# Kernel tuning notes

Hardware: AMD Instinct MI355X
Metric: run time of the kernel (lower is better)

Reference implementation:

```python
import jax, jax.numpy as jnp
import numpy as np

LN_EPS = 1e-5
TOP_K = 2


def _layernorm(x, g, b):
    mu = jnp.mean(x, axis=-1, keepdims=True)
    var = jnp.var(x, axis=-1, keepdims=True)
    return (x - mu) * jax.lax.rsqrt(var + LN_EPS) * g + b


def _moe_layer(x, ln_g, ln_b, Wr, br, We, be):
    # x: [B,T,H]; Wr: [H,E]; We: [E,H,H]; be: [E,H]
    E = Wr.shape[-1]
    z = _layernorm(x, ln_g, ln_b)
    logits = jnp.einsum('bth,he->bte', z, Wr) + br
    probs = jax.nn.softmax(logits, axis=-1)
    # top-k masking + renormalization (top_k < num_experts)
    topv, topi = jax.lax.top_k(probs, TOP_K)                      # [B,T,K]
    mask = (jax.nn.one_hot(topi, E, dtype=probs.dtype) * topv[..., None]).sum(-2)  # [B,T,E]
    w = mask / jnp.clip(mask.sum(-1, keepdims=True), 1e-8)
    # dense all-expert compute (faithful to torch.stack over experts), masked combine
    outs = jnp.einsum('bth,ehd->bted', z, We) + be                # [B,T,E,H]
    mixed = jnp.einsum('bte,bted->btd', w, outs)
    return x + mixed


def setup_inputs() -> dict:
    key = jax.random.key(0)
    B, T, H, E, L = 4, 2048, 3072, 4, 2
    ks = jax.random.split(key, 4)
    s = 1.0 / np.sqrt(H)
    x = jax.random.normal(ks[0], (B, T, H), dtype=jnp.float32)
    ln_g = jnp.ones((L, H), jnp.float32)
    ln_b = jnp.zeros((L, H), jnp.float32)
    Wr = jax.random.normal(ks[1], (L, H, E), jnp.float32) * s
    br = jnp.zeros((L, E), jnp.float32)
    We = jax.random.normal(ks[2], (L, E, H, H), jnp.float32) * s
    be = jnp.zeros((L, E, H), jnp.float32)
    return {"x": x, "ln_g": ln_g, "ln_b": ln_b, "Wr": Wr, "br": br, "We": We, "be": be}


def reference(x, ln_g, ln_b, Wr, br, We, be):
    L = ln_g.shape[0]
    for i in range(L):  # fixed small layer count
        x = _moe_layer(x, ln_g[i], ln_b[i], Wr[i], br[i], We[i], be[i])
    return x
```

## Files before the change

### kernel.cpp

```cpp
#include <hip/hip_runtime.h>
#include <hip/hip_bf16.h>
#include <stdint.h>

#define H 3072
#define EXPERTS 4
#define MTOK 8192
#define LN_EPS 1e-5f
#define FLAG_CAP 1024
#define TAU 0.03f
#define NT_MAX 70

#define BM 128
#define BN 128
#define BK 32

typedef __bf16 bf16;
typedef __bf16 bf16x8 __attribute__((ext_vector_type(8)));
typedef __bf16 bf16x4 __attribute__((ext_vector_type(4)));
typedef float  f32x4  __attribute__((ext_vector_type(4)));

typedef const __attribute__((address_space(1))) unsigned char* gas1p;
typedef __attribute__((address_space(3))) unsigned char* las3p;

__device__ __forceinline__ void gload_lds16(const void* g, void* l) {
    __builtin_amdgcn_global_load_lds((gas1p)g, (las3p)l, 16, 0, 0);
}

__device__ __forceinline__ int pair_a(int b) { return b < 3 ? 0 : (b < 5 ? 1 : 2); }
__device__ __forceinline__ int pair_b(int b) { return b < 3 ? b + 1 : (b < 5 ? b - 1 : 3); }

template <int WLO>
__global__ __launch_bounds__(256) void we_transpose(const float* __restrict__ We,
                                                    bf16* __restrict__ Wt_hi,
                                                    bf16* __restrict__ Wt_lo) {
    __shared__ float tile[64][65];
    const int e  = blockIdx.z;
    const int k0 = blockIdx.y * 64;
    const int n0 = blockIdx.x * 64;
    const int tid = threadIdx.x;

    const float* src = We + ((size_t)e * H + k0) * H + n0;
    const int kl = tid >> 4;
    const int nl = (tid & 15) * 4;
#pragma unroll
    for (int it = 0; it < 4; ++it) {
        float4 v = *(const float4*)(src + (size_t)(kl + it * 16) * H + nl);
        tile[kl + it * 16][nl + 0] = v.x;
        tile[kl + it * 16][nl + 1] = v.y;
        tile[kl + it * 16][nl + 2] = v.z;
        tile[kl + it * 16][nl + 3] = v.w;
    }
    __syncthreads();
    const size_t dbase = ((size_t)e * H + n0) * H + k0;
    const int nl2 = tid >> 4;
    const int kl2 = (tid & 15) * 4;
#pragma unroll
    for (int it = 0; it < 4; ++it) {
        bf16x4 oh, ol;
#pragma unroll
        for (int j = 0; j < 4; ++j) {
            float v = tile[kl2 + j][nl2 + it * 16];
            bf16 hi = (bf16)v;
            oh[j] = hi;
            ol[j] = (bf16)(v - (float)hi);
        }
        const size_t doff = dbase + (size_t)(nl2 + it * 16) * H + kl2;
        *(bf16x4*)(Wt_hi + doff) = oh;
        if (WLO) *(bf16x4*)(Wt_lo + doff) = ol;
    }
}

template <int MODE>
__global__ __launch_bounds__(256) void ln_router_k(const float* __restrict__ xin,
                                                   const float* __restrict__ gamma,
                                                   const float* __restrict__ beta,
                                                   const float* __restrict__ Wr,
                                                   const float* __restrict__ br,
                                                   bf16* __restrict__ z,
                                                   float* __restrict__ wout,
                                                   int* __restrict__ bkt,
                                                   int* __restrict__ bcount,
                                                   int* __restrict__ flags) {
    __shared__ float red[4][4];
    __shared__ float bc[2];

    const int t    = blockIdx.x;
    const int tid  = threadIdx.x;
    const int wid  = tid >> 6;
    const int lane = tid & 63;
    const float* xrow = xin + (size_t)t * H;

    float4 xv[3];
    float s = 0.f;
#pragma unroll
    for (int c = 0; c < 3; ++c) {
        xv[c] = *(const float4*)(xrow + (c * 256 + tid) * 4);
        s += xv[c].x + xv[c].y + xv[c].z + xv[c].w;
    }
#pragma unroll
    for (int off = 32; off; off >>= 1) s += __shfl_down(s, off);
    if (lane == 0) red[wid][0] = s;
    __syncthreads();
    if (tid == 0) bc[0] = (red[0][0] + red[1][0] + red[2][0] + red[3][0]) * (1.f / (float)H);
    __syncthreads();
    const float mu = bc[0];

    float d = 0.f;
#pragma unroll
    for (int c = 0; c < 3; ++c) {
        float dx;
        dx = xv[c].x - mu; d += dx * dx;
        dx = xv[c].y - mu; d += dx * dx;
        dx = xv[c].z - mu; d += dx * dx;
        dx = xv[c].w - mu; d += dx * dx;
    }
#pragma unroll
    for (int off = 32; off; off >>= 1) d += __shfl_down(d, off);
    if (lane == 0) red[wid][1] = d;
    __syncthreads();
    if (tid == 0) {
        float var = (red[0][1] + red[1][1] + red[2][1] + red[3][1]) * (1.f / (float)H);
        bc[1] = 1.f / sqrtf(var + LN_EPS);
    }
    __syncthreads();
    const float rs = bc[1];

    float l0 = 0.f, l1 = 0.f, l2 = 0.f, l3 = 0.f;
    bf16* zrow = z + (size_t)t * H;
#pragma unroll
    for (int c = 0; c < 3; ++c) {
        const int i0 = (c * 256 + tid) * 4;
        float4 gv = *(const float4*)(gamma + i0);
        float4 bv = *(const float4*)(beta + i0);
        float zz[4];
        zz[0] = (xv[c].x - mu) * rs * gv.x + bv.x;
        zz[1] = (xv[c].y - mu) * rs * gv.y + bv.y;
        zz[2] = (xv[c].z - mu) * rs * gv.z + bv.z;
        zz[3] = (xv[c].w - mu) * rs * gv.w + bv.w;
        if (MODE == 0) {
            bf16x4 zb = { (bf16)zz[0], (bf16)zz[1], (bf16)zz[2], (bf16)zz[3] };
            *(bf16x4*)(zrow + i0) = zb;
        }
#pragma unroll
        for (int j = 0; j < 4; ++j) {
            float4 wr = *(const float4*)(Wr + (size_t)(i0 + j) * 4);
            l0 += zz[j] * wr.x; l1 += zz[j] * wr.y;
            l2 += zz[j] * wr.z; l3 += zz[j] * wr.w;
        }
    }
    __syncthreads();
#pragma unroll
    for (int off = 32; off; off >>= 1) {
        l0 += __shfl_down(l0, off);
        l1 += __shfl_down(l1, off);
        l2 += __shfl_down(l2, off);
        l3 += __shfl_down(l3, off);
    }
    if (lane == 0) { red[wid][0] = l0; red[wid][1] = l1; red[wid][2] = l2; red[wid][3] = l3; }
    __syncthreads();
    if (tid == 0) {
        float lf[4];
#pragma unroll
        for (int e = 0; e < 4; ++e)
            lf[e] = red[0][e] + red[1][e] + red[2][e] + red[3][e] + br[e];
        if (MODE == 0) {
            float mx = fmaxf(fmaxf(lf[0], lf[1]), fmaxf(lf[2], lf[3]));
            float p[4]; float ps = 0.f;
#pragma unroll
            for (int e = 0; e < 4; ++e) { p[e] = expf(lf[e] - mx); ps += p[e]; }
#pragma unroll
            for (int e = 0; e < 4; ++e) p[e] /= ps;
            int i1 = 0; float v1 = p[0];
#pragma unroll
            for (int e = 1; e < 4; ++e) if (p[e] > v1) { v1 = p[e]; i1 = e; }
            int i2 = -1; float v2 = -1.f;
#pragma unroll
            for (int e = 0; e < 4; ++e) if (e != i1 && p[e] > v2) { v2 = p[e]; i2 = e; }
            const float den = fmaxf(v1 + v2, 1e-8f);
            float w4[4] = {0.f, 0.f, 0.f, 0.f};
            w4[i1] = v1 / den;
            w4[i2] = v2 / den;
            *(float4*)(wout + (size_t)t * 4) = make_float4(w4[0], w4[1], w4[2], w4[3]);
            const int lo = min(i1, i2), hi = max(i1, i2);
            const int b = (lo == 0) ? hi - 1 : (lo == 1 ? hi + 1 : 5);
            bkt[t] = b;
            atomicAdd(&bcount[b], 1);
        } else {
            float a = lf[0], b = lf[1], c = lf[2], dd = lf[3], t1;
#define SW_(p,q) if (p < q) { t1 = p; p = q; q = t1; }
            SW_(a, b) SW_(c, dd) SW_(a, c) SW_(b, dd) SW_(b, c)
#undef SW_
            if (b - c < TAU) {
                int idx = atomicAdd(flags, 1);
                if (idx < FLAG_CAP) flags[1 + idx] = t;
            }
        }
    }
}

__global__ void zero_flags(int* flags) { if (threadIdx.x == 0) flags[0] = 0; }
__global__ void zero12(int* bcount) { if (threadIdx.x < 12) bcount[threadIdx.x] = 0; }

__global__ __launch_bounds__(256) void bucket_scan(const int* __restrict__ bcount,
                                                   int* __restrict__ off_g,
                                                   int* __restrict__ tile_bkt,
                                                   int* __restrict__ tile_end,
                                                   int* __restrict__ tokslot) {
    for (int i = threadIdx.x; i < NT_MAX * BM; i += 256) tokslot[i] = 0;
    if (threadIdx.x == 0) {
        int off = 0, tile = 0;
        for (int b = 0; b < 6; ++b) {
            off_g[b] = off;
            const int c = bcount[b];
            const int ntb = (c + BM - 1) / BM;
            for (int k = 0; k < ntb; ++k) { tile_bkt[tile] = b; tile_end[tile] = off + c; ++tile; }
            off += ntb * BM;
        }
        for (; tile < NT_MAX; ++tile) { tile_bkt[tile] = -1; tile_end[tile] = 0; }
    }
}

__global__ __launch_bounds__(256) void scatter(const int* __restrict__ bkt,
                                               const int* __restrict__ off_g,
                                               int* __restrict__ cursor,
                                               int* __restrict__ tokslot,
                                               int* __restrict__ slot_of) {
    const int t = blockIdx.x * 256 + threadIdx.x;
    if (t >= MTOK) return;
    const int b = bkt[t];
    const int slot = off_g[b] + atomicAdd(&cursor[b], 1);
    tokslot[slot] = t;
    slot_of[t] = slot;
}

__global__ __launch_bounds__(384) void scatter_scale(const bf16* __restrict__ z,
                                                     const float* __restrict__ wb,
                                                     const int* __restrict__ bkt,
                                                     const int* __restrict__ slot_of,
                                                     bf16* __restrict__ zA,
                                                     bf16* __restrict__ zB) {
    const int t = blockIdx.x;
    const int b = bkt[t];
    const float wa = wb[(size_t)t * 4 + pair_a(b)];
    const float wv = wb[(size_t)t * 4 + pair_b(b)];
    const size_t slot = (size_t)slot_of[t];
    const int i0 = threadIdx.x * 8;
    const bf16x8 v = *(const bf16x8*)(z + (size_t)t * H + i0);
    bf16x8 ra, rb;
#pragma unroll
    for (int j = 0; j < 8; ++j) {
        const float f = (float)v[j];
        ra[j] = (bf16)(f * wa);
        rb[j] = (bf16)(f * wv);
    }
    *(bf16x8*)(zA + slot * H + i0) = ra;
    *(bf16x8*)(zB + slot * H + i0) = rb;
}

__global__ __launch_bounds__(256) void zfill(const float* __restrict__ x,
                                             const float* __restrict__ gamma,
                                             const float* __restrict__ beta,
                                             const int* __restrict__ flags,
                                             const float* __restrict__ wb,
                                             bf16* __restrict__ zc_hi,
                                             bf16* __restrict__ zc_lo,
                                             float* __restrict__ wfo) {
    __shared__ float red[4][2];
    __shared__ float bc[2];
    const int i = blockIdx.x;
    int count = flags[0]; if (count > FLAG_CAP) count = FLAG_CAP;
    if (i >= count) return;
    const int t = flags[1 + i];
    const int tid = threadIdx.x, wid = tid >> 6, lane = tid & 63;
    const float* xrow = x + (size_t)t * H;

    float4 xv[3]; float s = 0.f;
#pragma unroll
    for (int c = 0; c < 3; ++c) {
        xv[c] = *(const float4*)(xrow + (c * 256 + tid) * 4);
        s += xv[c].x + xv[c].y + xv[c].z + xv[c].w;
    }
#pragma unroll
    for (int off = 32; off; off >>= 1) s += __shfl_down(s, off);
    if (lane == 0) red[wid][0] = s;
    __syncthreads();
    if (tid == 0) bc[0] = (red[0][0] + red[1][0] + red[2][0] + red[3][0]) * (1.f / (float)H);
    __syncthreads();
    const float mu = bc[0];
    float d = 0.f;
#pragma unroll
    for (int c = 0; c < 3; ++c) {
        float dx;
        dx = xv[c].x - mu; d += dx * dx;
        dx = xv[c].y - mu; d += dx * dx;
        dx = xv[c].z - mu; d += dx * dx;
        dx = xv[c].w - mu; d += dx * dx;
    }
#pragma unroll
    for (int off = 32; off; off >>= 1) d += __shfl_down(d, off);
    if (lane == 0) red[wid][1] = d;
    __syncthreads();
    if (tid == 0) bc[1] = 1.f / sqrtf((red[0][1] + red[1][1] + red[2][1] + red[3][1]) * (1.f / (float)H) + LN_EPS);
    __syncthreads();
    const float rs = bc[1];

    bf16* zh = zc_hi + (size_t)i * H;
    bf16* zl = zc_lo + (size_t)i * H;
#pragma unroll
    for (int c = 0; c < 3; ++c) {
        const int i0 = (c * 256 + tid) * 4;
        float4 gv = *(const float4*)(gamma + i0);
        float4 bv = *(const float4*)(beta + i0);
        float vv[4];
        vv[0] = (xv[c].x - mu) * rs * gv.x + bv.x;
        vv[1] = (xv[c].y - mu) * rs * gv.y + bv.y;
        vv[2] = (xv[c].z - mu) * rs * gv.z + bv.z;
        vv[3] = (xv[c].w - mu) * rs * gv.w + bv.w;
        bf16x4 oh, ol;
#pragma unroll
        for (int j = 0; j < 4; ++j) {
            bf16 hi = (bf16)vv[j];
            oh[j] = hi;
            ol[j] = (bf16)(vv[j] - (float)hi);
        }
        *(bf16x4*)(zh + i0) = oh;
        *(bf16x4*)(zl + i0) = ol;
    }
    if (tid == 0) *(float4*)(wfo + (size_t)i * 4) = *(const float4*)(wb + (size_t)t * 4);
}

__global__ __launch_bounds__(256) void refine_mfma(const bf16* __restrict__ zc_hi,
                                                   const bf16* __restrict__ zc_lo,
                                                   const bf16* __restrict__ Wt_hi,
                                                   const bf16* __restrict__ Wt_lo,
                                                   const float* __restrict__ wf,
                                                   const float* __restrict__ be,
                                                   const int* __restrict__ flags,
                                                   float* __restrict__ partial) {
    int count = flags[0]; if (count > FLAG_CAP) count = FLAG_CAP;
    const int tileM = blockIdx.y * BM;
    if (tileM >= count) return;
    const int e = blockIdx.z;

    __shared__ __align__(16) bf16 Ah[2][BM * BK];
    __shared__ __align__(16) bf16 Al[2][BM * BK];
    __shared__ __align__(16) bf16 Bh[2][BN * BK];
    __shared__ __align__(16) bf16 Bl[2][BN * BK];
    __shared__ float wlds[BM];

    const int tid  = threadIdx.x;
    const int wid  = tid >> 6;
    const int lane = tid & 63;
    const int wm   = wid >> 1;
    const int wn   = wid & 1;
    const int tileN = blockIdx.x * BN;

    if (tid < 128) wlds[tid] = wf[(size_t)(tileM + tid) * 4 + e];

    const int srow   = lane >> 2;
    const int schunk = (((lane & 3) ^ ((lane >> 3) & 3)) * 8);
    const int lrow   = lane & 15;
    const int rchunk = (((lane >> 4) ^ ((lane >> 1) & 3)) * 8);
    const int r0   = wm * 64 + (lane >> 4) * 4;
    const int c0   = tileN + wn * 64 + (lane & 15);

    const bf16* Ahb = zc_hi;
    const bf16* Alb = zc_lo;
    const bf16* Bhb = Wt_hi + ((size_t)e * H + tileN) * H;
    const bf16* Blb = Wt_lo + ((size_t)e * H + tileN) * H;

#define RSTAGE(buf, kk0)                                                              \
    _Pragma("unroll")                                                                 \
    for (int i_ = 0; i_ < 2; ++i_) {                                                  \
        const int rr_ = wid * 32 + i_ * 16;                                           \
        gload_lds16(Ahb + (size_t)(tileM + rr_ + srow) * H + (kk0) + schunk,          \
                    &Ah[buf][(size_t)rr_ * BK]);                                      \
        gload_lds16(Alb + (size_t)(tileM + rr_ + srow) * H + (kk0) + schunk,          \
                    &Al[buf][(size_t)rr_ * BK]);                                      \
        gload_lds16(Bhb + (size_t)(rr_ + srow) * H + (kk0) + schunk,                  \
                    &Bh[buf][(size_t)rr_ * BK]);                                      \
        gload_lds16(Blb + (size_t)(rr_ + srow) * H + (kk0) + schunk,                  \
                    &Bl[buf][(size_t)rr_ * BK]);                                      \
    }

    f32x4 acc[4][4];
#pragma unroll
    for (int m = 0; m < 4; ++m)
#pragma unroll
        for (int n = 0; n < 4; ++n)
            acc[m][n] = (f32x4){0.f, 0.f, 0.f, 0.f};

    RSTAGE(0, 0)
    __syncthreads();

    int cur = 0;
    for (int kk = 0; kk < H / BK; ++kk) {
        if (kk + 1 < H / BK) { RSTAGE(cur ^ 1, (kk + 1) * BK) }

        bf16x8 ah[4], al[4], bh[4], bl[4];
#pragma unroll
        for (int m = 0; m < 4; ++m) {
            ah[m] = *(const bf16x8*)&Ah[cur][(wm * 64 + m * 16 + lrow) * BK + rchunk];
            al[m] = *(const bf16x8*)&Al[cur][(wm * 64 + m * 16 + lrow) * BK + rchunk];
        }
#pragma unroll
        for (int n = 0; n < 4; ++n) {
            bh[n] = *(const bf16x8*)&Bh[cur][(wn * 64 + n * 16 + lrow) * BK + rchunk];
            bl[n] = *(const bf16x8*)&Bl[cur][(wn * 64 + n * 16 + lrow) * BK + rchunk];
        }
#pragma unroll
        for (int m = 0; m < 4; ++m)
#pragma unroll
            for (int n = 0; n < 4; ++n) {
                acc[m][n] = __builtin_amdgcn_mfma_f32_16x16x32_bf16(al[m], bh[n], acc[m][n], 0, 0, 0);
                acc[m][n] = __builtin_amdgcn_mfma_f32_16x16x32_bf16(ah[m], bl[n], acc[m][n], 0, 0, 0);
                acc[m][n] = __builtin_amdgcn_mfma_f32_16x16x32_bf16(ah[m], bh[n], acc[m][n], 0, 0, 0);
            }
        __syncthreads();
        cur ^= 1;
    }
#undef RSTAGE

    float bev[4];
#pragma unroll
    for (int n = 0; n < 4; ++n)
        bev[n] = be[(size_t)e * H + c0 + n * 16];

#pragma unroll
    for (int m = 0; m < 4; ++m) {
#pragma unroll
        for (int r = 0; r < 4; ++r) {
            const int tl = r0 + m * 16 + r;
            const int g = tileM + tl;
            if (g < count) {
                const float w = wlds[tl];
                float* prow = partial + ((size_t)e * FLAG_CAP + g) * H;
#pragma unroll
                for (int n = 0; n < 4; ++n)
                    prow[c0 + n * 16] = w * (acc[m][n][r] + bev[n]);
            }
        }
    }
}

__global__ __launch_bounds__(256) void refine_combine(const float* __restrict__ partial,
                                                      const float* __restrict__ x,
                                                      const int* __restrict__ flags,
                                                      float* __restrict__ out) {
    int count = flags[0]; if (count > FLAG_CAP) count = FLAG_CAP;
    const int i = blockIdx.x;
    if (i >= count) return;
    const int t = flags[1 + i];
    const int tid = threadIdx.x;
#pragma unroll
    for (int c = 0; c < 3; ++c) {
        const int col = (c * 256 + tid) * 4;
        float4 s = *(const float4*)(x + (size_t)t * H + col);
#pragma unroll
        for (int e = 0; e < 4; ++e) {
            float4 p = *(const float4*)(partial + ((size_t)e * FLAG_CAP + i) * H + col);
            s.x += p.x; s.y += p.y; s.z += p.z; s.w += p.w;
        }
        *(float4*)(out + (size_t)t * H + col) = s;
    }
}

__global__ __launch_bounds__(256, 3) void moe_gemm_b(const bf16* __restrict__ zA,
                                                     const bf16* __restrict__ zB,
                                                     const bf16* __restrict__ Wt,
                                                     const int* __restrict__ tokslot,
                                                     const float* __restrict__ wbuf,
                                                     const int* __restrict__ tile_bkt,
                                                     const int* __restrict__ tile_end,
                                                     const float* __restrict__ xin,
                                                     const float* __restrict__ be,
                                                     float* __restrict__ out) {
    const int tile = blockIdx.y;
    const int b = tile_bkt[tile];
    if (b < 0) return;
    const int ea = pair_a(b);
    const int eb = pair_b(b);
    const int endSlot = tile_end[tile];

    __shared__ __align__(16) bf16 As[BM * BK];
    __shared__ __align__(16) bf16 Bs[BN * BK];
    __shared__ __align__(16) float wlds[BM * 4];
    __shared__ int tlds[BM];

    const int tid  = threadIdx.x;
    const int wid  = tid >> 6;
    const int lane = tid & 63;
    const int wm   = wid >> 1;
    const int wn   = wid & 1;
    const int tileM = tile * BM;
    const int tileN = blockIdx.x * BN;

    if (tid < 128) {
        const int tk = tokslot[tileM + tid];
        tlds[tid] = tk;
        *(float4*)&wlds[tid * 4] = *(const float4*)(wbuf + (size_t)tk * 4);
    }

    const int srow   = lane >> 2;
    const int schunk = (((lane & 3) ^ ((lane >> 3) & 3)) * 8);
    const int lrow   = lane & 15;
    const int rchunk = (((lane >> 4) ^ ((lane >> 1) & 3)) * 8);
    const int r0   = wm * 64 + (lane >> 4) * 4;
    const int c0   = tileN + wn * 64 + (lane & 15);

    f32x4 acc[4][4];
#pragma unroll
    for (int m = 0; m < 4; ++m)
#pragma unroll
        for (int n = 0; n < 4; ++n)
            acc[m][n] = (f32x4){0.f, 0.f, 0.f, 0.f};

    for (int ph = 0; ph < 2; ++ph) {
        const bf16* Asrc = ph ? zB : zA;
        const int ex = ph ? eb : ea;
        const bf16* Bbase = Wt + ((size_t)ex * H + tileN) * H;

        for (int k0 = 0; k0 < H; k0 += BK) {
            __syncthreads();
#pragma unroll
            for (int i = 0; i < 2; ++i) {
                const int rr = wid * 32 + i * 16;
                gload_lds16(Asrc + (size_t)(tileM + rr + srow) * H + k0 + schunk,
                            As + (size_t)rr * BK);
                gload_lds16(Bbase + (size_t)(rr + srow) * H + k0 + schunk,
                            Bs + (size_t)rr * BK);
            }
            __syncthreads();

            bf16x8 a[4], bfr[4];
#pragma unroll
            for (int m = 0; m < 4; ++m)
                a[m] = *(const bf16x8*)&As[(wm * 64 + m * 16 + lrow) * BK + rchunk];
#pragma unroll
            for (int n = 0; n < 4; ++n)
                bfr[n] = *(const bf16x8*)&Bs[(wn * 64 + n * 16 + lrow) * BK + rchunk];
#pragma unroll
            for (int m = 0; m < 4; ++m)
#pragma unroll
                for (int n = 0; n < 4; ++n)
                    acc[m][n] = __builtin_amdgcn_mfma_f32_16x16x32_bf16(a[m], bfr[n], acc[m][n], 0, 0, 0);
        }
    }

    float bev[4][4];
#pragma unroll
    for (int n = 0; n < 4; ++n)
#pragma unroll
        for (int e = 0; e < 4; ++e)
            bev[n][e] = be[(size_t)e * H + c0 + n * 16];

#pragma unroll
    for (int m = 0; m < 4; ++m) {
#pragma unroll
        for (int r = 0; r < 4; ++r) {
            const int tl = r0 + m * 16 + r;
            const int slotg = tileM + tl;
            if (slotg < endSlot) {
                const size_t t = (size_t)tlds[tl];
                const float4 wq = *(const float4*)&wlds[tl * 4];
                const float* xr = xin + t * H;
                float* orow = out + t * H;
#pragma unroll
                for (int n = 0; n < 4; ++n) {
                    const int col = c0 + n * 16;
                    const float bias = wq.x * bev[n][0] + wq.y * bev[n][1] +
                                       wq.z * bev[n][2] + wq.w * bev[n][3];
                    orow[col] = xr[col] + acc[m][n][r] + bias;
                }
            }
        }
    }
}

extern "C" void kernel_launch(void* const* d_in, const int* in_sizes, int n_in,
                              void* d_out, int out_size, void* d_ws, size_t ws_size,
                              hipStream_t stream) {
    (void)in_sizes; (void)n_in; (void)out_size; (void)ws_size;

    const float* x    = (const float*)d_in[0];
    const float* ln_g = (const float*)d_in[1];
    const float* ln_b = (const float*)d_in[2];
    const float* Wr   = (const float*)d_in[3];
    const float* br   = (const float*)d_in[4];
    const float* We   = (const float*)d_in[5];
    const float* be   = (const float*)d_in[6];
    float* out = (float*)d_out;

    uint8_t* ws = (uint8_t*)d_ws;
    const size_t zBytes   = (size_t)MTOK * H * 2;
    const size_t wtBytes  = (size_t)EXPERTS * H * H * 2;
    const size_t wbBytes  = (size_t)MTOK * 4 * 4;
    const size_t zcBytes  = (size_t)FLAG_CAP * H * 2;
    const size_t wfBytes  = (size_t)(FLAG_CAP + 128) * 4 * 4;
    const size_t flgBytes = 8192;
    const size_t zsBytes  = (size_t)NT_MAX * BM * H * 2;

    bf16*  z    = (bf16*)ws;                                       ws += zBytes;
    bf16*  WtH  = (bf16*)ws;                                       ws += wtBytes;
    bf16*  WtL  = (bf16*)ws;                                       ws += wtBytes;
    float* wb   = (float*)ws;                                      ws += wbBytes;
    bf16*  zcH  = (bf16*)ws;                                       ws += zcBytes;
    bf16*  zcL  = (bf16*)ws;                                       ws += zcBytes;
    float* wf   = (float*)ws;                                      ws += wfBytes;
    int*   flg  = (int*)ws;                                        ws += flgBytes;
    bf16*  zA   = (bf16*)ws;                                       ws += zsBytes;
    bf16*  zB   = (bf16*)ws;                                       ws += zsBytes;
    int*   bkt  = (int*)ws;                                        ws += (size_t)MTOK * 4;
    int*   slot_of = (int*)ws;                                     ws += (size_t)MTOK * 4;
    int*   tokslot = (int*)ws;                                     ws += (size_t)NT_MAX * BM * 4;
    int*   bcount  = (int*)ws;                                     ws += 256;
    int*   off_g   = (int*)ws;                                     ws += 256;
    int*   tile_bkt = (int*)ws;                                    ws += 1024;
    int*   tile_end = (int*)ws;                                    ws += 1024;
    int*   cursor = bcount + 6;
    float* partial = (float*)zA;

    const dim3 gemm_grid(H / BN, NT_MAX);

    we_transpose<1><<<dim3(H / 64, H / 64, EXPERTS), 256, 0, stream>>>(We, WtH, WtL);
    zero12<<<1, 64, 0, stream>>>(bcount);
    ln_router_k<0><<<dim3(MTOK), 256, 0, stream>>>(x, ln_g, ln_b, Wr, br, z, wb, bkt, bcount, flg);
    bucket_scan<<<1, 256, 0, stream>>>(bcount, off_g, tile_bkt, tile_end, tokslot);
    scatter<<<dim3(MTOK / 256), 256, 0, stream>>>(bkt, off_g, cursor, tokslot, slot_of);
    scatter_scale<<<dim3(MTOK), 384, 0, stream>>>(z, wb, bkt, slot_of, zA, zB);
    moe_gemm_b<<<gemm_grid, 256, 0, stream>>>(zA, zB, WtH, tokslot, wb, tile_bkt, tile_end, x, be, out);

    zero_flags<<<1, 64, 0, stream>>>(flg);
    ln_router_k<1><<<dim3(MTOK), 256, 0, stream>>>(out, ln_g + H, ln_b + H,
                                                   Wr + (size_t)H * EXPERTS, br + EXPERTS,
                                                   z, wb, bkt, bcount, flg);
    zfill<<<dim3(FLAG_CAP), 256, 0, stream>>>(x, ln_g, ln_b, flg, wb, zcH, zcL, wf);
    refine_mfma<<<dim3(H / BN, FLAG_CAP / BM, EXPERTS), 256, 0, stream>>>(zcH, zcL, WtH, WtL,
                                                                          wf, be, flg, partial);
    refine_combine<<<dim3(FLAG_CAP), 256, 0, stream>>>(partial, x, flg, out);

    we_transpose<0><<<dim3(H / 64, H / 64, EXPERTS), 256, 0, stream>>>(
        We + (size_t)EXPERTS * H * H, WtH, WtL);
    zero12<<<1, 64, 0, stream>>>(bcount);
    ln_router_k<0><<<dim3(MTOK), 256, 0, stream>>>(out, ln_g + H, ln_b + H,
                                                   Wr + (size_t)H * EXPERTS, br + EXPERTS,
                                                   z, wb, bkt, bcount, flg);
    bucket_scan<<<1, 256, 0, stream>>>(bcount, off_g, tile_bkt, tile_end, tokslot);
    scatter<<<dim3(MTOK / 256), 256, 0, stream>>>(bkt, off_g, cursor, tokslot, slot_of);
    scatter_scale<<<dim3(MTOK), 384, 0, stream>>>(z, wb, bkt, slot_of, zA, zB);
    moe_gemm_b<<<gemm_grid, 256, 0, stream>>>(zA, zB, WtH, tokslot, wb, tile_bkt, tile_end, out,
                                              be + (size_t)EXPERTS * H, out);
}
```

Measured before the change: 1.659 ms.

## Triple-buffer LDS loads in expert GEMM to overlap global loads with MFMA

Replaces the single-buffered load/sync/compute loop in moe_gemm_b with a three-stage LDS ring. Both expert phases are flattened into one stream of k-steps, and loads are issued two stages ahead. Explicit vmcnt waits and a single barrier per step replace the two syncthreads. The goal is to hide global-to-LDS latency behind MFMA work. In exchange it triples the LDS footprint, which may reduce occupancy at launch bounds of 3 blocks per CU.

```diff
diff --git a/kernel.cpp b/kernel.cpp
--- a/kernel.cpp
+++ b/kernel.cpp
@@ -13,6 +13,8 @@
 #define BM 128
 #define BN 128
 #define BK 32
+#define KSTEPS (H / BK)
+#define NS (2 * KSTEPS)
 
 typedef __bf16 bf16;
 typedef __bf16 bf16x8 __attribute__((ext_vector_type(8)));
@@ -482,8 +484,8 @@
     const int eb = pair_b(b);
     const int endSlot = tile_end[tile];
 
-    __shared__ __align__(16) bf16 As[BM * BK];
-    __shared__ __align__(16) bf16 Bs[BN * BK];
+    __shared__ __align__(16) bf16 As[3][BM * BK];
+    __shared__ __align__(16) bf16 Bs[3][BN * BK];
     __shared__ __align__(16) float wlds[BM * 4];
     __shared__ int tlds[BM];
 
@@ -508,6 +510,24 @@
     const int r0   = wm * 64 + (lane >> 4) * 4;
     const int c0   = tileN + wn * 64 + (lane & 15);
 
+    const bf16* BbaseA = Wt + ((size_t)ea * H + tileN) * H;
+    const bf16* BbaseB = Wt + ((size_t)eb * H + tileN) * H;
+
+#define GSTAGE(buf, vk)                                                               \
+    {                                                                                 \
+        const bf16* Asrc_  = ((vk) < KSTEPS) ? zA : zB;                               \
+        const bf16* Bbase_ = ((vk) < KSTEPS) ? BbaseA : BbaseB;                       \
+        const int k0_ = (((vk) < KSTEPS) ? (vk) : (vk) - KSTEPS) * BK;                \
+        _Pragma("unroll")                                                             \
+        for (int i_ = 0; i_ < 2; ++i_) {                                              \
+            const int rr_ = wid * 32 + i_ * 16;                                       \
+            gload_lds16(Asrc_ + (size_t)(tileM + rr_ + srow) * H + k0_ + schunk,      \
+                        &As[buf][(size_t)rr_ * BK]);                                  \
+            gload_lds16(Bbase_ + (size_t)(rr_ + srow) * H + k0_ + schunk,             \
+                        &Bs[buf][(size_t)rr_ * BK]);                                  \
+        }                                                                             \
+    }
+
     f32x4 acc[4][4];
 #pragma unroll
     for (int m = 0; m < 4; ++m)
@@ -515,37 +535,43 @@
         for (int n = 0; n < 4; ++n)
             acc[m][n] = (f32x4){0.f, 0.f, 0.f, 0.f};
 
-    for (int ph = 0; ph < 2; ++ph) {
-        const bf16* Asrc = ph ? zB : zA;
-        const int ex = ph ? eb : ea;
-        const bf16* Bbase = Wt + ((size_t)ex * H + tileN) * H;
-
-        for (int k0 = 0; k0 < H; k0 += BK) {
-            __syncthreads();
-#pragma unroll
-            for (int i = 0; i < 2; ++i) {
-                const int rr = wid * 32 + i * 16;
-                gload_lds16(Asrc + (size_t)(tileM + rr + srow) * H + k0 + schunk,
-                            As + (size_t)rr * BK);
-                gload_lds16(Bbase + (size_t)(rr + srow) * H + k0 + schunk,
-                            Bs + (size_t)rr * BK);
-            }
-            __syncthreads();
-
-            bf16x8 a[4], bfr[4];
-#pragma unroll
-            for (int m = 0; m < 4; ++m)
-                a[m] = *(const bf16x8*)&As[(wm * 64 + m * 16 + lrow) * BK + rchunk];
+    __syncthreads();
+    GSTAGE(0, 0)
+    GSTAGE(1, 1)
+    asm volatile("s_waitcnt vmcnt(4)" ::: "memory");
+    __builtin_amdgcn_sched_barrier(0);
+    __builtin_amdgcn_s_barrier();
+
+    for (int t = 0; t < NS; ++t) {
+        const int rb = t % 3;
+        bf16x8 a[4], bfr[4];
+#pragma unroll
+        for (int m = 0; m < 4; ++m)
+            a[m] = *(const bf16x8*)&As[rb][(wm * 64 + m * 16 + lrow) * BK + rchunk];
+#pragma unroll
+        for (int n = 0; n < 4; ++n)
+            bfr[n] = *(const bf16x8*)&Bs[rb][(wn * 64 + n * 16 + lrow) * BK + rchunk];
+
+        const bool haveStage = (t + 2 < NS);
+        if (haveStage) GSTAGE((t + 2) % 3, t + 2)
+
+#pragma unroll
+        for (int m = 0; m < 4; ++m)
 #pragma unroll
             for (int n = 0; n < 4; ++n)
-                bfr[n] = *(const bf16x8*)&Bs[(wn * 64 + n * 16 + lrow) * BK + rchunk];
-#pragma unroll
-            for (int m = 0; m < 4; ++m)
-#pragma unroll
-                for (int n = 0; n < 4; ++n)
-                    acc[m][n] = __builtin_amdgcn_mfma_f32_16x16x32_bf16(a[m], bfr[n], acc[m][n], 0, 0, 0);
-        }
-    }
+                acc[m][n] = __builtin_amdgcn_mfma_f32_16x16x32_bf16(a[m], bfr[n], acc[m][n], 0, 0, 0);
+
+        asm volatile("s_waitcnt lgkmcnt(0)" ::: "memory");
+        __builtin_amdgcn_sched_barrier(0);
+        if (haveStage) {
+            asm volatile("s_waitcnt vmcnt(4)" ::: "memory");
+        } else {
+            asm volatile("s_waitcnt vmcnt(0)" ::: "memory");
+        }
+        __builtin_amdgcn_sched_barrier(0);
+        __builtin_amdgcn_s_barrier();
+    }
+#undef GSTAGE
 
     float bev[4][4];
 #pragma unroll
```

Measured after the change: 1.628 ms. No clear change (-1.9%).
